# Kernel tuning notes

Hardware: AMD Instinct MI355X
Metric: run time of the kernel (lower is better)

## Reference

```python
import jax, jax.numpy as jnp
import numpy as np
import math

D_MODEL = 1024
D_STATE = 16
D_CONV = 4
EXPAND = 2
D_INNER = D_MODEL * EXPAND
BATCH = 2
SEQ = 2048


def setup_inputs() -> dict:
    key = jax.random.key(0)
    ks = jax.random.split(key, 8)
    s = 0.02
    x = jax.random.normal(ks[0], (BATCH, SEQ, D_MODEL), dtype=jnp.float32)
    in_proj_w = jax.random.normal(ks[1], (D_MODEL, 2 * D_INNER), dtype=jnp.float32) * s
    conv_w = jax.random.normal(ks[2], (D_INNER, D_CONV), dtype=jnp.float32) * s
    conv_b = jnp.zeros((D_INNER,), dtype=jnp.float32)
    x_proj_w = jax.random.normal(ks[3], (D_INNER, 2 * D_STATE + 1), dtype=jnp.float32) * s
    A_log = jnp.log(jnp.broadcast_to(jnp.arange(1, D_STATE + 1, dtype=jnp.float32)[None, :], (D_INNER, D_STATE)))
    dt_w = jax.random.normal(ks[4], (D_INNER, 1), dtype=jnp.float32) * s
    # special dt bias init: softplus^{-1}(dt_init)
    u = jax.random.uniform(ks[5], (D_INNER,), dtype=jnp.float32)
    dt_init = jnp.exp(u * (math.log(0.1) - math.log(0.001)) + math.log(0.001))
    dt_b = dt_init + jnp.log(-jnp.expm1(-dt_init))
    out_proj_w = jax.random.normal(ks[6], (D_INNER, D_MODEL), dtype=jnp.float32) * s
    ln_g = jnp.ones((D_MODEL,), dtype=jnp.float32)
    ln_b = jnp.zeros((D_MODEL,), dtype=jnp.float32)
    return {"x": x, "in_proj_w": in_proj_w, "conv_w": conv_w, "conv_b": conv_b,
            "x_proj_w": x_proj_w, "A_log": A_log, "dt_w": dt_w, "dt_b": dt_b,
            "out_proj_w": out_proj_w, "ln_g": ln_g, "ln_b": ln_b}


def _silu(x):
    return x * jax.nn.sigmoid(x)


def _layernorm(x, g, b, eps=1e-5):
    mu = jnp.mean(x, axis=-1, keepdims=True)
    var = jnp.mean(jnp.square(x - mu), axis=-1, keepdims=True)
    return (x - mu) * jax.lax.rsqrt(var + eps) * g + b


def _ssm_forward(x, in_proj_w, conv_w, conv_b, x_proj_w, A_log, dt_w, dt_b, out_proj_w, ln_g, ln_b):
    residual = x
    xn = _layernorm(x, ln_g, ln_b)
    xz = xn @ in_proj_w                      # (B, L, 2*d_inner)
    x_b, z = jnp.split(xz, 2, axis=-1)
    # causal depthwise conv1d (pad left d_conv-1, truncate to L)
    xc = jnp.transpose(x_b, (0, 2, 1))       # (B, d_inner, L)
    kern = conv_w[:, None, :]                # (d_inner, 1, K) OIH
    xc = jax.lax.conv_general_dilated(
        xc, kern, window_strides=(1,), padding=[(D_CONV - 1, 0)],
        dimension_numbers=("NCH", "OIH", "NCH"), feature_group_count=D_INNER)
    xc = xc + conv_b[None, :, None]
    x_b = _silu(jnp.transpose(xc, (0, 2, 1)))  # (B, L, d_inner)

    params = x_b @ x_proj_w                  # (B, L, 2*d_state+1)
    B_p = params[:, :, :D_STATE]             # (B, L, d_state)
    C_p = params[:, :, D_STATE:2 * D_STATE]  # (B, L, d_state)
    dt = jax.nn.softplus(params[:, :, -1:] * dt_w[:, 0][None, None, :] + dt_b)  # (B, L, d_inner)
    A = -jnp.exp(A_log)                      # (d_inner, d_state)

    # selective scan over time; per-step dA/dBu computed on the fly
    def step(h, inp):
        u_t, dt_t, B_t, C_t = inp            # (B,di),(B,di),(B,ds),(B,ds)
        dA = jnp.exp(dt_t[..., None] * A)    # (B, d_inner, d_state)
        h = dA * h + (dt_t * u_t)[..., None] * B_t[:, None, :]
        y = jnp.einsum('bds,bs->bd', h, C_t)
        return h, y

    xs = (jnp.swapaxes(x_b, 0, 1), jnp.swapaxes(dt, 0, 1),
          jnp.swapaxes(B_p, 0, 1), jnp.swapaxes(C_p, 0, 1))
    h0 = jnp.zeros((x.shape[0], D_INNER, D_STATE), dtype=x.dtype)
    _, ys = jax.lax.scan(step, h0, xs)       # ys: (L, B, d_inner)
    y = jnp.swapaxes(ys, 0, 1)

    y = y * _silu(z)
    return y @ out_proj_w + residual


def reference(x, in_proj_w, conv_w, conv_b, x_proj_w, A_log, dt_w, dt_b, out_proj_w, ln_g, ln_b):
    return _ssm_forward(x, in_proj_w, conv_w, conv_b, x_proj_w, A_log, dt_w, dt_b, out_proj_w, ln_g, ln_b)
```

## Files before the change

### kernel.cpp

```cpp
#include <hip/hip_runtime.h>
#include <stdint.h>


typedef short short8 __attribute__((ext_vector_type(8)));
typedef float f32x4 __attribute__((ext_vector_type(4)));

#define DEV static __device__ __forceinline__

constexpr int BATCH = 2, SEQ = 2048, DM = 1024, DI = 2048, NST = 16;
constexpr int NTOK = BATCH * SEQ;
constexpr int CH_NC = 64, CH_CL = 32;
constexpr int XP_SLICES = 4, XP_KS = 512;

DEV float bf2f(ushort h) {
    union { uint u; float f; } c; c.u = ((uint)h) << 16; return c.f;
}
DEV ushort f2bf(float x) {
    union { uint u; float f; } c; c.f = x;
    uint u = c.u;
    uint r = (u + 0x7FFFu + ((u >> 16) & 1u)) >> 16;
    return (ushort)r;
}
DEV float softplus_f(float arg) {
    return (arg > 15.f) ? arg : __logf(1.f + __expf(arg));
}
DEV float silu_f(float x) { return x / (1.f + __expf(-x)); }

DEV void stage16(const void* g, void* l) {
    __builtin_amdgcn_global_load_lds(
        (const __attribute__((address_space(1))) void*)g,
        (__attribute__((address_space(3))) void*)l,
        16, 0, 0);
}

__global__ __launch_bounds__(256) void prep_weights(const float* __restrict__ ipw,
                                                    const float* __restrict__ opw,
                                                    const float* __restrict__ xpw,
                                                    ushort* __restrict__ Bt1,
                                                    ushort* __restrict__ Bt2,
                                                    ushort* __restrict__ Wtx) {
    __shared__ float tile[32][33];
    int bid = blockIdx.x;
    int tid = threadIdx.x;
    if (bid < 6144) {
        const float* W; ushort* Bt; int K, N, bx, by;
        if (bid < 4096) { W = ipw; Bt = Bt1; K = 1024; N = 4096; bx = bid & 127; by = bid >> 7; }
        else { int b2 = bid - 4096; W = opw; Bt = Bt2; K = 2048; N = 1024; bx = b2 & 31; by = b2 >> 5; }
        int tx = tid & 31, ty = tid >> 5;
        int n0 = bx * 32, k0 = by * 32;
#pragma unroll
        for (int i = 0; i < 32; i += 8)
            tile[ty + i][tx] = W[(size_t)(k0 + ty + i) * N + n0 + tx];
        __syncthreads();
#pragma unroll
        for (int i = 0; i < 32; i += 8)
            Bt[(size_t)(n0 + ty + i) * K + k0 + tx] = f2bf(tile[tx][ty + i]);
    } else {
        int idx = (bid - 6144) * 256 + tid;
        int j = idx >> 11, k = idx & (DI - 1);
        Wtx[idx] = (j < 33) ? f2bf(xpw[(size_t)k * 33 + j]) : (ushort)0;
    }
}

__global__ __launch_bounds__(256) void ln_kernel(const float* __restrict__ x,
                                                 const float* __restrict__ g,
                                                 const float* __restrict__ b,
                                                 ushort* __restrict__ xn) {
    int row = blockIdx.x;
    int tid = threadIdx.x;
    const float4 v = ((const float4*)(x + (size_t)row * DM))[tid];
    float s = v.x + v.y + v.z + v.w;
    float sq = v.x * v.x + v.y * v.y + v.z * v.z + v.w * v.w;
#pragma unroll
    for (int o = 32; o; o >>= 1) { s += __shfl_down(s, o); sq += __shfl_down(sq, o); }
    __shared__ float ls[4], lsq[4];
    __shared__ float smu, srs;
    int wid = tid >> 6;
    if ((tid & 63) == 0) { ls[wid] = s; lsq[wid] = sq; }
    __syncthreads();
    if (tid == 0) {
        float S = ls[0] + ls[1] + ls[2] + ls[3];
        float SQ = lsq[0] + lsq[1] + lsq[2] + lsq[3];
        float mu = S / DM;
        float var = SQ / DM - mu * mu;
        smu = mu; srs = rsqrtf(var + 1e-5f);
    }
    __syncthreads();
    float mu = smu, rs = srs;
    const float4 gg = ((const float4*)g)[tid];
    const float4 bb = ((const float4*)b)[tid];
    ushort4 o;
    o.x = f2bf((v.x - mu) * rs * gg.x + bb.x);
    o.y = f2bf((v.y - mu) * rs * gg.y + bb.y);
    o.z = f2bf((v.z - mu) * rs * gg.z + bb.z);
    o.w = f2bf((v.w - mu) * rs * gg.w + bb.w);
    ((ushort4*)(xn + (size_t)row * DM))[tid] = o;
}

template <int WM, int WN, int BMW, int BNW, int SWZ_NRX, typename OUT_T, bool RES>
__global__ __launch_bounds__(WM * WN * 64, 2) void gemm_pipe(const ushort* __restrict__ A,
                                                             const ushort* __restrict__ Bt,
                                                             OUT_T* __restrict__ C,
                                                             const float* __restrict__ res,
                                                             int M, int N, int K,
                                                             int lda, int ldb) {
    constexpr int THREADS = WM * WN * 64;
    constexpr int BM = WM * BMW * 16, BN = WN * BNW * 16;
    constexpr int CR = THREADS / 8;
    constexpr int NLOADS = (BM + BN) / CR;
    extern __shared__ ushort lds[];

    int bxi, byi;
    if constexpr (SWZ_NRX > 0) {
        constexpr int NRX = SWZ_NRX, NRY = 8 / NRX;
        int gx = gridDim.x, gy = gridDim.y;
        int RR = gy / NRY, RC = gx / NRX;
        int lid = blockIdx.y * gx + blockIdx.x;
        int xcd = lid & 7, t = lid >> 3;
        byi = (xcd / NRX) * RR + (t % RR);
        bxi = (xcd % NRX) * RC + (t / RR);
    } else {
        bxi = blockIdx.x; byi = blockIdx.y;
    }

    int tid = threadIdx.x;
    int lane = tid & 63, w = tid >> 6;
    int wm = w / WN, wn = w % WN;
    int lr = lane & 15, kc = lane >> 4;
    int m0 = byi * BM, n0 = bxi * BN;
    int kbase = blockIdx.z * K;
    const ushort* Ag = A + (size_t)m0 * lda + kbase;
    const ushort* Bg = Bt + (size_t)n0 * ldb + kbase;
    C += (size_t)blockIdx.z * M * N;

    int r_in = tid >> 3;
    int sc = (((tid & 7) ^ (r_in & 7))) * 8;
    int lbase_off = 8 * w * 64;

    auto stage = [&](const ushort* gsrc, int ld, ushort* lbase, int nrows, int k0) {
#pragma unroll
        for (int c = 0; c < nrows; c += CR) {
            stage16(gsrc + (size_t)(c + r_in) * ld + k0 + sc,
                    lbase + (size_t)c * 64 + lbase_off);
        }
    };

    f32x4 acc[BMW][BNW];
#pragma unroll
    for (int i = 0; i < BMW; i++)
#pragma unroll
        for (int j = 0; j < BNW; j++) acc[i][j] = (f32x4){0.f, 0.f, 0.f, 0.f};

    const int NT = K >> 6;
    stage(Ag, lda, lds, BM, 0);
    stage(Bg, ldb, lds + BM * 64, BN, 0);

    for (int kt = 0; kt < NT; ++kt) {
        int p = kt & 1;
        ushort* bA = lds + (size_t)p * (BM + BN) * 64;
        ushort* bB = bA + BM * 64;
        ushort* nA = lds + (size_t)(p ^ 1) * (BM + BN) * 64;
        if (kt + 1 < NT) {
            stage(Ag, lda, nA, BM, (kt + 1) * 64);
            stage(Bg, ldb, nA + BM * 64, BN, (kt + 1) * 64);
            if constexpr (NLOADS == 4)
                asm volatile("s_waitcnt vmcnt(4)" ::: "memory");
            else if constexpr (NLOADS == 6)
                asm volatile("s_waitcnt vmcnt(6)" ::: "memory");
            else if constexpr (NLOADS == 8)
                asm volatile("s_waitcnt vmcnt(8)" ::: "memory");
            else
                asm volatile("s_waitcnt vmcnt(0)" ::: "memory");
        } else {
            asm volatile("s_waitcnt vmcnt(0)" ::: "memory");
        }
        __builtin_amdgcn_sched_barrier(0);
        __builtin_amdgcn_s_barrier();
        __builtin_amdgcn_sched_barrier(0);

        short8 af[BMW][2], bfr[BNW][2];
#pragma unroll
        for (int mi = 0; mi < BMW; mi++) {
            int row = wm * BMW * 16 + mi * 16 + lr;
#pragma unroll
            for (int kk = 0; kk < 2; kk++)
                af[mi][kk] = *(const short8*)(bA + (size_t)row * 64 + (((kk * 4 + kc) ^ (lr & 7)) * 8));
        }
#pragma unroll
        for (int ni = 0; ni < BNW; ni++) {
            int row = wn * BNW * 16 + ni * 16 + lr;
#pragma unroll
            for (int kk = 0; kk < 2; kk++)
                bfr[ni][kk] = *(const short8*)(bB + (size_t)row * 64 + (((kk * 4 + kc) ^ (lr & 7)) * 8));
        }
        __builtin_amdgcn_s_setprio(1);
#pragma unroll
        for (int kk = 0; kk < 2; kk++)
#pragma unroll
            for (int mi = 0; mi < BMW; mi++)
#pragma unroll
                for (int ni = 0; ni < BNW; ni++)
                    acc[mi][ni] = __builtin_amdgcn_mfma_f32_16x16x32_bf16(af[mi][kk], bfr[ni][kk], acc[mi][ni], 0, 0, 0);
        __builtin_amdgcn_s_setprio(0);
        __builtin_amdgcn_sched_barrier(0);
        __builtin_amdgcn_s_barrier();
        __builtin_amdgcn_sched_barrier(0);
    }

#pragma unroll
    for (int mi = 0; mi < BMW; mi++) {
        int r = m0 + wm * BMW * 16 + mi * 16 + kc * 4;
#pragma unroll
        for (int ni = 0; ni < BNW; ni++) {
            int cc = n0 + wn * BNW * 16 + ni * 16 + lr;
#pragma unroll
            for (int j = 0; j < 4; j++) {
                float v = acc[mi][ni][j];
                size_t off = (size_t)(r + j) * N + cc;
                if (RES) v += res[off];
                if constexpr (sizeof(OUT_T) == 2) C[off] = f2bf(v);
                else C[off] = v;
            }
        }
    }
}

__global__ __launch_bounds__(256) void conv_silu(const ushort* __restrict__ xz,
                                                 const float* __restrict__ cw,
                                                 const float* __restrict__ cb,
                                                 ushort* __restrict__ u,
                                                 ushort* __restrict__ szg) {
    int blk = blockIdx.x;
    int b = blk >> 8;
    int t0 = (blk & 255) * 8;
    int d0 = threadIdx.x * 8;

    float4 wreg[8];
#pragma unroll
    for (int j = 0; j < 8; j++) wreg[j] = *(const float4*)(cw + (size_t)(d0 + j) * 4);
    float breg[8];
#pragma unroll
    for (int j = 0; j < 8; j++) breg[j] = cb[d0 + j];

    const short8 zero8 = (short8){0, 0, 0, 0, 0, 0, 0, 0};
    auto loadx = [&](int t) -> short8 {
        if (t < 0) return zero8;
        return *(const short8*)(xz + (size_t)(b * SEQ + t) * (2 * DI) + d0);
    };
    short8 ta = loadx(t0 - 3), tb_ = loadx(t0 - 2), tc = loadx(t0 - 1);
#pragma unroll
    for (int i = 0; i < 8; i++) {
        int row = b * SEQ + t0 + i;
        short8 td = *(const short8*)(xz + (size_t)row * (2 * DI) + d0);
        short8 zv = *(const short8*)(xz + (size_t)row * (2 * DI) + DI + d0);
        short8 u8, sz8;
#pragma unroll
        for (int j = 0; j < 8; j++) {
            float acc = breg[j];
            acc = fmaf(bf2f((ushort)ta[j]), wreg[j].x, acc);
            acc = fmaf(bf2f((ushort)tb_[j]), wreg[j].y, acc);
            acc = fmaf(bf2f((ushort)tc[j]), wreg[j].z, acc);
            acc = fmaf(bf2f((ushort)td[j]), wreg[j].w, acc);
            u8[j] = (short)f2bf(silu_f(acc));
            sz8[j] = (short)f2bf(silu_f(bf2f((ushort)zv[j])));
        }
        *(short8*)(u + (size_t)row * DI + d0) = u8;
        *(short8*)(szg + (size_t)row * DI + d0) = sz8;
        ta = tb_; tb_ = tc; tc = td;
    }
}

__global__ __launch_bounds__(256) void xproj_reduce(const float* __restrict__ part,
                                                    float* __restrict__ params) {
    int i = blockIdx.x * 256 + threadIdx.x;
    const f32x4* p = (const f32x4*)part;
    constexpr size_t SL = (size_t)NTOK * 64 / 4;
    f32x4 s = p[i] + p[SL + i] + p[2 * SL + i] + p[3 * SL + i];
    ((f32x4*)params)[i] = s;
}

DEV void scan_decode(int bid, int tid, int& b, int& chunk, int& d) {
    int lane = tid & 63;
    int w = __builtin_amdgcn_readfirstlane(tid >> 6);
    b = bid >> 9;
    int dg = (bid >> 4) & 31;
    int cq = bid & 15;
    chunk = cq * 4 + w;
    d = dg * 64 + lane;
}

__global__ __launch_bounds__(256) void scan_part1(const ushort* __restrict__ u,
                                                  const float* __restrict__ params,
                                                  const float* __restrict__ A_log,
                                                  const float* __restrict__ dt_w,
                                                  const float* __restrict__ dt_b,
                                                  ushort* __restrict__ hst,
                                                  float* __restrict__ sdt) {
    int b, chunk, d;
    scan_decode(blockIdx.x, threadIdx.x, b, chunk, d);
    float dtw = dt_w[d], dtbv = dt_b[d];
    float a[16];
#pragma unroll
    for (int s = 0; s < 16; s++) a[s] = -__expf(A_log[(size_t)d * 16 + s]);
    float h[16];
#pragma unroll
    for (int s = 0; s < 16; s++) h[s] = 0.f;
    float sumdt = 0.f;
    int row0 = b * SEQ + chunk * CH_CL;
#pragma unroll 4
    for (int t = 0; t < CH_CL; t++) {
        int row = row0 + t;
        const float* pr = params + (size_t)row * 64;
        float uu = bf2f(u[(size_t)row * DI + d]);
        float dt = softplus_f(fmaf(pr[32], dtw, dtbv));
        sumdt += dt;
        float du = dt * uu;
        const f32x4* Bp = (const f32x4*)pr;
        f32x4 B0 = Bp[0], B1 = Bp[1], B2 = Bp[2], B3 = Bp[3];
#pragma unroll
        for (int r = 0; r < 4; r++) {
            h[r]      = fmaf(h[r],      __expf(dt * a[r]),      du * B0[r]);
            h[4 + r]  = fmaf(h[4 + r],  __expf(dt * a[4 + r]),  du * B1[r]);
            h[8 + r]  = fmaf(h[8 + r],  __expf(dt * a[8 + r]),  du * B2[r]);
            h[12 + r] = fmaf(h[12 + r], __expf(dt * a[12 + r]), du * B3[r]);
        }
    }
    ushort* hp = hst + (((size_t)(b * CH_NC + chunk) * DI + d) << 4);
    short8 ho[2];
#pragma unroll
    for (int s = 0; s < 16; s++) ho[s >> 3][s & 7] = (short)f2bf(h[s]);
    *(short8*)hp = ho[0];
    *(short8*)(hp + 8) = ho[1];
    sdt[(size_t)(b * CH_NC + chunk) * DI + d] = sumdt;
}

__global__ __launch_bounds__(256) void scan_stitch(const float* __restrict__ A_log,
                                                   ushort* __restrict__ hst,
                                                   const float* __restrict__ sdt) {
    int idx = blockIdx.x * 256 + threadIdx.x;
    int s = idx & 15, d = (idx >> 4) & (DI - 1), b = idx >> 15;
    float a = -__expf(A_log[(size_t)d * 16 + s]);
    float carry = 0.f;
    for (int c = 0; c < CH_NC; c++) {
        size_t o = (((size_t)(b * CH_NC + c) * DI + d) << 4) + s;
        float prev = carry;
        carry = fmaf(carry, __expf(a * sdt[(size_t)(b * CH_NC + c) * DI + d]), bf2f(hst[o]));
        hst[o] = f2bf(prev);
    }
}

__global__ __launch_bounds__(256) void scan_part2(const ushort* __restrict__ u,
                                                  const float* __restrict__ params,
                                                  const float* __restrict__ A_log,
                                                  const float* __restrict__ dt_w,
                                                  const float* __restrict__ dt_b,
                                                  const ushort* __restrict__ hst,
                                                  const ushort* __restrict__ szg,
                                                  ushort* __restrict__ yg) {
    int b, chunk, d;
    scan_decode(blockIdx.x, threadIdx.x, b, chunk, d);
    float dtw = dt_w[d], dtbv = dt_b[d];
    float a[16];
#pragma unroll
    for (int s = 0; s < 16; s++) a[s] = -__expf(A_log[(size_t)d * 16 + s]);
    const ushort* hp = hst + (((size_t)(b * CH_NC + chunk) * DI + d) << 4);
    short8 hi0 = *(const short8*)hp;
    short8 hi1 = *(const short8*)(hp + 8);
    float h[16];
#pragma unroll
    for (int s = 0; s < 16; s++) h[s] = bf2f((ushort)(s < 8 ? hi0[s] : hi1[s - 8]));
    int row0 = b * SEQ + chunk * CH_CL;
#pragma unroll 4
    for (int t = 0; t < CH_CL; t++) {
        int row = row0 + t;
        const float* pr = params + (size_t)row * 64;
        float uu = bf2f(u[(size_t)row * DI + d]);
        float dt = softplus_f(fmaf(pr[32], dtw, dtbv));
        float du = dt * uu;
        const f32x4* Bp = (const f32x4*)pr;
        const f32x4* Cp = (const f32x4*)(pr + 16);
        f32x4 B0 = Bp[0], B1 = Bp[1], B2 = Bp[2], B3 = Bp[3];
        f32x4 C0 = Cp[0], C1 = Cp[1], C2 = Cp[2], C3 = Cp[3];
        float y = 0.f;
#pragma unroll
        for (int r = 0; r < 4; r++) {
            h[r]      = fmaf(h[r],      __expf(dt * a[r]),      du * B0[r]);
            h[4 + r]  = fmaf(h[4 + r],  __expf(dt * a[4 + r]),  du * B1[r]);
            h[8 + r]  = fmaf(h[8 + r],  __expf(dt * a[8 + r]),  du * B2[r]);
            h[12 + r] = fmaf(h[12 + r], __expf(dt * a[12 + r]), du * B3[r]);
            y += h[r] * C0[r] + h[4 + r] * C1[r] + h[8 + r] * C2[r] + h[12 + r] * C3[r];
        }
        float sz = bf2f(szg[(size_t)row * DI + d]);
        yg[(size_t)row * DI + d] = f2bf(y * sz);
    }
}

extern "C" void kernel_launch(void* const* d_in, const int* in_sizes, int n_in,
                              void* d_out, int out_size, void* d_ws, size_t ws_size,
                              hipStream_t stream) {
    const float* x    = (const float*)d_in[0];
    const float* ipw  = (const float*)d_in[1];
    const float* cw   = (const float*)d_in[2];
    const float* cb   = (const float*)d_in[3];
    const float* xpw  = (const float*)d_in[4];
    const float* alog = (const float*)d_in[5];
    const float* dtw  = (const float*)d_in[6];
    const float* dtb  = (const float*)d_in[7];
    const float* opw  = (const float*)d_in[8];
    const float* lng  = (const float*)d_in[9];
    const float* lnb  = (const float*)d_in[10];
    float* out = (float*)d_out;

    char* ws = (char*)d_ws;
    size_t off = 0;
    auto carve = [&](size_t bytes) -> void* {
        void* p = ws + off;
        off = (off + bytes + 255) & ~(size_t)255;
        return p;
    };
    ushort* Bt1  = (ushort*)carve((size_t)4096 * 1024 * 2);
    ushort* Bt2  = (ushort*)carve((size_t)1024 * 2048 * 2);
    ushort* Wtx  = (ushort*)carve((size_t)64 * DI * 2);
    ushort* xn   = (ushort*)carve((size_t)NTOK * DM * 2);
    ushort* xz   = (ushort*)carve((size_t)NTOK * 2 * DI * 2);
    ushort* u    = (ushort*)carve((size_t)NTOK * DI * 2);
    ushort* szg  = (ushort*)carve((size_t)NTOK * DI * 2);
    float*  params = (float*)carve((size_t)NTOK * 64 * 4);
    ushort* hst  = (ushort*)carve((size_t)BATCH * CH_NC * DI * NST * 2);
    float*  sdt  = (float*) carve((size_t)BATCH * CH_NC * DI * 4);
    ushort* yg   = (ushort*)carve((size_t)NTOK * DI * 2);
    float*  part = (float*)yg;

    prep_weights<<<6656, 256, 0, stream>>>(ipw, opw, xpw, Bt1, Bt2, Wtx);
    ln_kernel<<<NTOK, 256, 0, stream>>>(x, lng, lnb, xn);
    gemm_pipe<2, 2, 4, 4, 2, ushort, false>
        <<<dim3(32, 32, 1), 256, 2 * (128 + 128) * 64 * sizeof(ushort), stream>>>(
            xn, Bt1, xz, nullptr, NTOK, 4096, 1024, 1024, 1024);
    conv_silu<<<512, 256, 0, stream>>>(xz, cw, cb, u, szg);
    gemm_pipe<2, 2, 2, 2, 0, float, false>
        <<<dim3(1, 64, XP_SLICES), 256, 2 * (64 + 64) * 64 * sizeof(ushort), stream>>>(
            u, Wtx, part, nullptr, NTOK, 64, XP_KS, DI, DI);
    xproj_reduce<<<(NTOK * 64 / 4) / 256, 256, 0, stream>>>(part, params);
    scan_part1<<<1024, 256, 0, stream>>>(u, params, alog, dtw, dtb, hst, sdt);
    scan_stitch<<<(BATCH * DI * NST) / 256, 256, 0, stream>>>(alog, hst, sdt);
    scan_part2<<<1024, 256, 0, stream>>>(u, params, alog, dtw, dtb, hst, szg, yg);
    gemm_pipe<2, 2, 2, 4, 0, float, true>
        <<<dim3(8, 64, 1), 256, 2 * (64 + 128) * 64 * sizeof(ushort), stream>>>(
            yg, Bt2, out, x, NTOK, 1024, 2048, 2048, 2048);
}
```

Before: 172.8 us.

## Use 256x256-tile 8-wave GEMM kernel for in_proj

Adds a dedicated in_proj GEMM kernel with 256x256 output tiles, 8 waves of 512 threads, a double-buffered LDS pipeline, and phased MFMA issue under raised wave priority. It also remaps block IDs so each XCD works on a contiguous sub-grid. The aim is more operand reuse per LDS byte and better L2 locality than the previous 128x128 tile kernel. In exchange it uses 128KB of LDS per block and a 256-block grid (one block per CU), adds a barrier per phase, and holds a 128-float accumulator per thread, which raises register pressure.

Result: slower. 177.5 us (+2.7%).

```diff
diff --git a/kernel.cpp b/kernel.cpp
--- a/kernel.cpp
+++ b/kernel.cpp
@@ -95,6 +95,113 @@
     o.z = f2bf((v.z - mu) * rs * gg.z + bb.z);
     o.w = f2bf((v.w - mu) * rs * gg.w + bb.w);
     ((ushort4*)(xn + (size_t)row * DM))[tid] = o;
+}
+
+__global__ __launch_bounds__(512, 2) void gemm_pipe8(const ushort* __restrict__ A,
+                                                     const ushort* __restrict__ Bt,
+                                                     ushort* __restrict__ C,
+                                                     int M, int N, int K,
+                                                     int lda, int ldb) {
+    extern __shared__ ushort lds[];
+
+    int gx = gridDim.x;
+    int RR = gridDim.y / 4, RC = gx / 2;
+    int lid = blockIdx.y * gx + blockIdx.x;
+    int xcd = lid & 7, t = lid >> 3;
+    int byi = (xcd >> 1) * RR + (t % RR);
+    int bxi = (xcd & 1) * RC + (t / RR);
+
+    int tid = threadIdx.x;
+    int lane = tid & 63, w = tid >> 6;
+    int wm = w >> 2, wn = w & 3;
+    int lr = lane & 15, kc = lane >> 4;
+    int m0 = byi * 256, n0 = bxi * 256;
+    const ushort* Ag = A + (size_t)m0 * lda;
+    const ushort* Bg = Bt + (size_t)n0 * ldb;
+
+    int r_in = tid >> 3;
+    int sc = (((tid & 7) ^ (r_in & 7))) * 8;
+    int lbase_off = 8 * w * 64;
+
+    auto stage = [&](const ushort* gsrc, int ld, ushort* lbase, int k0) {
+#pragma unroll
+        for (int c = 0; c < 256; c += 64) {
+            stage16(gsrc + (size_t)(c + r_in) * ld + k0 + sc,
+                    lbase + (size_t)c * 64 + lbase_off);
+        }
+    };
+
+    f32x4 acc[8][4];
+#pragma unroll
+    for (int i = 0; i < 8; i++)
+#pragma unroll
+        for (int j = 0; j < 4; j++) acc[i][j] = (f32x4){0.f, 0.f, 0.f, 0.f};
+
+    const int NT = K >> 6;
+    stage(Ag, lda, lds, 0);
+    stage(Bg, ldb, lds + 256 * 64, 0);
+
+    for (int kt = 0; kt < NT; ++kt) {
+        int p = kt & 1;
+        ushort* bA = lds + (size_t)p * 512 * 64;
+        ushort* bB = bA + 256 * 64;
+        ushort* nA = lds + (size_t)(p ^ 1) * 512 * 64;
+        if (kt + 1 < NT) {
+            stage(Ag, lda, nA, (kt + 1) * 64);
+            stage(Bg, ldb, nA + 256 * 64, (kt + 1) * 64);
+            asm volatile("s_waitcnt vmcnt(8)" ::: "memory");
+        } else {
+            asm volatile("s_waitcnt vmcnt(0)" ::: "memory");
+        }
+        __builtin_amdgcn_sched_barrier(0);
+        __builtin_amdgcn_s_barrier();
+        __builtin_amdgcn_sched_barrier(0);
+
+#pragma unroll
+        for (int ph = 0; ph < 4; ++ph) {
+            const int qm = ph >> 1, qn = ph & 1;
+            short8 af[4][2], bf_[2][2];
+#pragma unroll
+            for (int mi2 = 0; mi2 < 4; mi2++) {
+                int row = wm * 128 + (qm * 4 + mi2) * 16 + lr;
+#pragma unroll
+                for (int kk = 0; kk < 2; kk++)
+                    af[mi2][kk] = *(const short8*)(bA + (size_t)row * 64 + (((kk * 4 + kc) ^ (lr & 7)) * 8));
+            }
+#pragma unroll
+            for (int ni2 = 0; ni2 < 2; ni2++) {
+                int row = wn * 64 + (qn * 2 + ni2) * 16 + lr;
+#pragma unroll
+                for (int kk = 0; kk < 2; kk++)
+                    bf_[ni2][kk] = *(const short8*)(bB + (size_t)row * 64 + (((kk * 4 + kc) ^ (lr & 7)) * 8));
+            }
+            __builtin_amdgcn_s_setprio(1);
+#pragma unroll
+            for (int kk = 0; kk < 2; kk++)
+#pragma unroll
+                for (int mi2 = 0; mi2 < 4; mi2++)
+#pragma unroll
+                    for (int ni2 = 0; ni2 < 2; ni2++)
+                        acc[qm * 4 + mi2][qn * 2 + ni2] = __builtin_amdgcn_mfma_f32_16x16x32_bf16(
+                            af[mi2][kk], bf_[ni2][kk], acc[qm * 4 + mi2][qn * 2 + ni2], 0, 0, 0);
+            __builtin_amdgcn_s_setprio(0);
+            __builtin_amdgcn_sched_barrier(0);
+            __builtin_amdgcn_s_barrier();
+            __builtin_amdgcn_sched_barrier(0);
+        }
+    }
+
+#pragma unroll
+    for (int mi = 0; mi < 8; mi++) {
+        int r = m0 + wm * 128 + mi * 16 + kc * 4;
+#pragma unroll
+        for (int ni = 0; ni < 4; ni++) {
+            int cc = n0 + wn * 64 + ni * 16 + lr;
+#pragma unroll
+            for (int j = 0; j < 4; j++)
+                C[(size_t)(r + j) * N + cc] = f2bf(acc[mi][ni][j]);
+        }
+    }
 }
 
 template <int WM, int WN, int BMW, int BNW, int SWZ_NRX, typename OUT_T, bool RES>
@@ -433,9 +540,8 @@
 
     prep_weights<<<6656, 256, 0, stream>>>(ipw, opw, xpw, Bt1, Bt2, Wtx);
     ln_kernel<<<NTOK, 256, 0, stream>>>(x, lng, lnb, xn);
-    gemm_pipe<2, 2, 4, 4, 2, ushort, false>
-        <<<dim3(32, 32, 1), 256, 2 * (128 + 128) * 64 * sizeof(ushort), stream>>>(
-            xn, Bt1, xz, nullptr, NTOK, 4096, 1024, 1024, 1024);
+    gemm_pipe8<<<dim3(16, 16), 512, 2 * 512 * 64 * sizeof(ushort), stream>>>(
+        xn, Bt1, xz, NTOK, 4096, 1024, 1024, 1024);
     conv_silu<<<512, 256, 0, stream>>>(xz, cw, cb, u, szg);
     gemm_pipe<2, 2, 2, 2, 0, float, false>
         <<<dim3(1, 64, XP_SLICES), 256, 2 * (64 + 64) * 64 * sizeof(ushort), stream>>>(
```
